# Optimization experiments

Measured on AMD Instinct MI355X. Metric: run time of the kernel, lower is better.

The kernel has to match this reference:

```python
import jax, jax.numpy as jnp
import numpy as np
from jax import lax

ED = 192      # mambapy d_inner = 2 * d_model(Ci=96)
N = 16        # d_state
DT_RANK = 6   # ceil(96/16)
DCONV1 = 4    # mambapy causal conv1d kernel
CI = 96

def _rms(x, w):
    return x * lax.rsqrt(jnp.mean(x * x, axis=-1, keepdims=True) + 1e-5) * w

def _mamba_layer(u, p):
    # u: [B, L, CI]; one mambapy ResidualBlock (RMSNorm -> MambaBlock -> +residual)
    (rms_w, m_in_w, m_conv_w, m_conv_b, x_proj_w, dt_proj_w, dt_proj_b,
     A_log, D_param, m_out_w) = p
    xn = _rms(u, rms_w)
    xz = xn @ m_in_w.T                      # [B,L,2*ED]
    xm, z = jnp.split(xz, 2, axis=-1)
    # causal depthwise conv1d (torch pads d_conv-1 both sides then slices [:L])
    xc = lax.conv_general_dilated(jnp.swapaxes(xm, 1, 2), m_conv_w, (1,),
                                  [(DCONV1 - 1, 0)],
                                  dimension_numbers=('NCH', 'OIH', 'NCH'),
                                  feature_group_count=ED) + m_conv_b[None, :, None]
    xm = jax.nn.silu(jnp.swapaxes(xc, 1, 2))  # [B,L,ED]
    dbc = xm @ x_proj_w.T                     # [B,L,dt_rank+2N]
    dt = dbc[..., :DT_RANK]
    Bm = dbc[..., DT_RANK:DT_RANK + N]
    Cm = dbc[..., DT_RANK + N:]
    delta = jax.nn.softplus(dt @ dt_proj_w.T + dt_proj_b)   # [B,L,ED]
    A = -jnp.exp(A_log)                                      # [ED,N]
    dA = jnp.exp(delta[..., None] * A)                       # [B,L,ED,N]
    dBx = (delta * xm)[..., None] * Bm[:, :, None, :]        # [B,L,ED,N]
    def comb(c1, c2):
        a1, b1 = c1
        a2, b2 = c2
        return a1 * a2, a2 * b1 + b2
    _, h = lax.associative_scan(comb, (dA, dBx), axis=1)     # h: [B,L,ED,N]
    y = jnp.einsum('blen,bln->ble', h, Cm) + D_param * xm
    y = y * jax.nn.silu(z)
    return u + y @ m_out_w.T

def _seq(x3d, p):
    # x3d: [B, C', H, W, D] -> flatten spatial to L, run mamba, reshape back
    B, C, H, W, D = x3d.shape
    xs = jnp.swapaxes(x3d.reshape(B, C, H * W * D), 1, 2)
    ys = _mamba_layer(xs, p)  # mamba_layers = 1
    return jnp.swapaxes(ys, 1, 2).reshape(B, C, H, W, D)

def setup_inputs() -> dict:
    key = jax.random.key(0)
    ks = jax.random.split(key, 12)
    B, H, W, D, C = 1, 16, 16, 16, 96
    s = 0.05
    return {
        'x': jax.random.normal(ks[0], (B, H, W, D, C), jnp.float32),
        'in_proj_w': jax.random.normal(ks[1], (CI, C), jnp.float32) * s,
        'conv3d_w': jax.random.normal(ks[2], (CI, 1, 3, 3, 3), jnp.float32) * s,
        'conv3d_b': jax.random.normal(ks[3], (CI,), jnp.float32) * s,
        'rms_w': jnp.ones((CI,), jnp.float32),
        'm_in_w': jax.random.normal(ks[4], (2 * ED, CI), jnp.float32) * s,
        'm_conv_w': jax.random.normal(ks[5], (ED, 1, DCONV1), jnp.float32) * s,
        'm_conv_b': jax.random.normal(ks[6], (ED,), jnp.float32) * s,
        'x_proj_w': jax.random.normal(ks[7], (DT_RANK + 2 * N, ED), jnp.float32) * s,
        'dt_proj_w': jax.random.normal(ks[8], (ED, DT_RANK), jnp.float32) * s,
        'dt_proj_b': jax.random.uniform(ks[9], (ED,), jnp.float32, -4.0, -2.0),
        'A_log': jnp.log(jnp.tile(jnp.arange(1, N + 1, dtype=jnp.float32), (ED, 1))),
        'D_param': jnp.ones((ED,), jnp.float32),
        'm_out_w': jax.random.normal(ks[10], (CI, ED), jnp.float32) * s,
        'ln_g': jnp.ones((CI,), jnp.float32),
        'ln_b': jnp.zeros((CI,), jnp.float32),
        'out_proj_w': jax.random.normal(ks[11], (C, CI), jnp.float32) * s,
    }

def reference(x, in_proj_w, conv3d_w, conv3d_b, rms_w, m_in_w, m_conv_w, m_conv_b,
              x_proj_w, dt_proj_w, dt_proj_b, A_log, D_param, m_out_w,
              ln_g, ln_b, out_proj_w):
    p = (rms_w, m_in_w, m_conv_w, m_conv_b, x_proj_w, dt_proj_w, dt_proj_b,
         A_log, D_param, m_out_w)
    h = x @ in_proj_w.T                               # [B,H,W,D,Ci]
    xcf = jnp.transpose(h, (0, 4, 1, 2, 3))           # channel-first
    xcf = lax.conv_general_dilated(xcf, conv3d_w, (1, 1, 1), [(1, 1)] * 3,
                                   dimension_numbers=('NCHWD', 'OIHWD', 'NCHWD'),
                                   feature_group_count=CI) \
          + conv3d_b[None, :, None, None, None]
    xcf = jax.nn.silu(xcf)
    x0 = xcf                                          # orientation 0: rot = identity
    x1 = jnp.swapaxes(x0, 2, 4)
    x2 = jnp.swapaxes(x0, 3, 4)
    flip = lambda a: jnp.flip(a, (2, 3, 4))
    y0 = _seq(x0, p) + flip(_seq(flip(x0), p))
    y1 = _seq(x1, p) + flip(_seq(flip(x1), p))
    y2 = _seq(x2, p) + flip(_seq(flip(x2), p))
    y = y0 + jnp.swapaxes(y1, 2, 4) + jnp.swapaxes(y2, 3, 4)
    ycl = jnp.transpose(y, (0, 2, 3, 4, 1))           # channel-last
    mu = jnp.mean(ycl, -1, keepdims=True)
    var = jnp.var(ycl, -1, keepdims=True)
    ycl = (ycl - mu) * lax.rsqrt(var + 1e-5) * ln_g + ln_b
    return ycl @ out_proj_w.T
```

## Files before the change

kernel.cpp:

```cpp
#include <hip/hip_runtime.h>
#include <hip/hip_fp16.h>
#include <math.h>

static constexpr int LSEQ = 4096;
static constexpr int ED_  = 192;
static constexpr int NS   = 16;
static constexpr int NC   = 128;
static constexpr int LC   = 32;
static constexpr int XMS  = 196;
static constexpr int WDS  = 196;

__device__ __forceinline__ float d_silu(float x){ return x / (1.f + __expf(-x)); }
__device__ __forceinline__ float d_softplus(float x){
  return fmaxf(x, 0.f) + __logf(1.f + __expf(-fabsf(x)));
}

__device__ __forceinline__ int vox_of(int l, int ord, int dir){
  int m = dir ? (LSEQ-1-l) : l;
  if(ord==0) return m;
  int a=(m>>8)&15, b=(m>>4)&15, c=m&15;
  if(ord==1) return (c<<8)|(b<<4)|a;
  return (a<<8)|(c<<4)|b;
}

__global__ __launch_bounds__(256) void k_inproj(const float* __restrict__ x, const float* __restrict__ w,
                                                float* __restrict__ hbuf){
  __shared__ float wl[96*104];
  __shared__ float xr[16*100];
  int t = threadIdx.x;
  for(int idx=t; idx<9216; idx+=256){ int o=idx/96, c=idx%96; wl[o*104+c] = w[idx]; }
  int vb = blockIdx.x*16;
  for(int idx=t; idx<1536; idx+=256){ int vv=idx/96, c=idx%96; xr[vv*100+c] = x[(vb+vv)*96 + c]; }
  __syncthreads();
  for(int r=0;r<6;r++){
    int idx = t + 256*r;
    int o = idx>>4, vsub = idx&15;
    const float* xrow = xr + vsub*100;
    const float* wrow = wl + o*104;
    float4 s4 = {0.f,0.f,0.f,0.f};
    #pragma unroll
    for(int c4=0;c4<24;c4++){
      float4 a = *(const float4*)(xrow + c4*4);
      float4 b = *(const float4*)(wrow + c4*4);
      s4.x += a.x*b.x; s4.y += a.y*b.y; s4.z += a.z*b.z; s4.w += a.w*b.w;
    }
    hbuf[(vb+vsub)*96 + o] = (s4.x+s4.y)+(s4.z+s4.w);
  }
}

__global__ __launch_bounds__(256) void k_conv3d(const float* __restrict__ hbuf, const float* __restrict__ w3,
                                                const float* __restrict__ b3, float* __restrict__ x0){
  __shared__ float w3l[96*27];
  __shared__ float b3l[96];
  int t = threadIdx.x;
  for(int idx=t; idx<2592; idx+=256) w3l[idx] = w3[idx];
  if(t<96) b3l[t] = b3[t];
  __syncthreads();
  int idx = blockIdx.x*256 + t;
  int vq = idx/96, c = idx%96;
  int h = vq>>6, wq = (vq>>2)&15, dq = vq&3, d0 = dq*4;
  float acc[4];
  float bb = b3l[c];
  acc[0]=bb; acc[1]=bb; acc[2]=bb; acc[3]=bb;
  for(int i=0;i<3;i++){ int hh=h+i-1; if((unsigned)hh>15u) continue;
    for(int j=0;j<3;j++){ int ww=wq+j-1; if((unsigned)ww>15u) continue;
      float val[6];
      #pragma unroll
      for(int tt=0;tt<6;tt++){
        int dd = d0 + tt - 1;
        val[tt] = ((unsigned)dd<=15u) ? hbuf[(((hh<<4)|ww)<<4|dd)*96 + c] : 0.f;
      }
      const float* wr = w3l + c*27 + i*9 + j*3;
      #pragma unroll
      for(int m=0;m<4;m++)
        acc[m] += val[m]*wr[0] + val[m+1]*wr[1] + val[m+2]*wr[2];
    }}
  int vbase = (((h<<4)|wq)<<4) | d0;
  #pragma unroll
  for(int m=0;m<4;m++) x0[(vbase+m)*96 + c] = d_silu(acc[m]);
}

__global__ __launch_bounds__(256) void k_rms(const float* __restrict__ x0, const float* __restrict__ rms_w,
                                             const float* __restrict__ m_in_w,
                                             float* __restrict__ xmpre, float* __restrict__ szb){
  __shared__ float wl[128*104];
  __shared__ float xn[16*100];
  int t = threadIdx.x;
  int wv = t>>6, lane = t&63;
  int quad = lane>>4, c = lane&15;
  int vsub = wv*4 + quad;
  int v = blockIdx.x*16 + vsub;
  const float* row = x0 + v*96;
  float a[6]; float ssq = 0.f;
  #pragma unroll
  for(int k=0;k<6;k++){ a[k] = row[c+16*k]; ssq += a[k]*a[k]; }
  #pragma unroll
  for(int o=8;o>0;o>>=1) ssq += __shfl_xor(ssq, o, 64);
  float r = rsqrtf(ssq*(1.f/96.f)+1e-5f);
  #pragma unroll
  for(int k=0;k<6;k++) xn[vsub*100 + c + 16*k] = a[k]*r*rms_w[c+16*k];
  for(int tile=0;tile<3;tile++){
    __syncthreads();
    for(int idx=t; idx<12288; idx+=256){ int rr=idx/96, cc=idx%96; wl[rr*104+cc] = m_in_w[(tile*128+rr)*96 + cc]; }
    __syncthreads();
    for(int rpt=0;rpt<8;rpt++){
      int idx = t + 256*rpt;
      int rloc = idx>>4, vs = idx&15;
      int e = tile*128 + rloc;
      const float* xrow = xn + vs*100;
      const float* wrow = wl + rloc*104;
      float4 s4={0.f,0.f,0.f,0.f};
      #pragma unroll
      for(int c4=0;c4<24;c4++){
        float4 aa = *(const float4*)(xrow+c4*4);
        float4 bb = *(const float4*)(wrow+c4*4);
        s4.x+=aa.x*bb.x; s4.y+=aa.y*bb.y; s4.z+=aa.z*bb.z; s4.w+=aa.w*bb.w;
      }
      float dsum = (s4.x+s4.y)+(s4.z+s4.w);
      int vg = blockIdx.x*16 + vs;
      if(e<ED_) xmpre[vg*ED_+e] = dsum;
      else      szb[vg*ED_+(e-ED_)] = d_silu(dsum);
    }
  }
}

__global__ __launch_bounds__(768,6) void kA(
    const float* __restrict__ xmpre,
    const float* __restrict__ mcw, const float* __restrict__ mcb,
    const float* __restrict__ xpw, const float* __restrict__ dtw, const float* __restrict__ dtb,
    const float* __restrict__ Dp,
    __half2* __restrict__ yS, float* __restrict__ hend, float* __restrict__ dbcC){
  __shared__ float s_xm[LC*XMS];
  __shared__ float s_dbc[LC*40];
  __shared__ float s_wdl[38*WDS];
  __shared__ int   vtab[36];
  int s = blockIdx.y, ord = s>>1, dir = s&1;
  int chunk = blockIdx.x, l0 = chunk*LC;
  int tid = threadIdx.x;
  for(int idx=tid; idx<38*192; idx+=768){ int j=idx/192, c=idx-j*192; s_wdl[j*WDS+c] = xpw[idx]; }
  if(tid < 35){
    int l = l0 - 3 + tid;
    vtab[tid] = (l>=0) ? vox_of(l, ord, dir) : 0;
  }
  __syncthreads();
  {
    int g = tid/192, e = tid - g*192;
    float4 wc = *(const float4*)(mcw + e*4);
    float bc = mcb[e];
    int lbase = l0 + 8*g;
    float h0=0.f, h1=0.f, h2=0.f;
    {
      int l = lbase-3; if(l>=0) h0 = xmpre[vtab[8*g+0]*ED_ + e];
      l = lbase-2;     if(l>=0) h1 = xmpre[vtab[8*g+1]*ED_ + e];
      l = lbase-1;     if(l>=0) h2 = xmpre[vtab[8*g+2]*ED_ + e];
    }
    #pragma unroll
    for(int i=0;i<8;i++){
      float cur = xmpre[vtab[8*g+3+i]*ED_ + e];
      float a = bc + h0*wc.x + h1*wc.y + h2*wc.z + cur*wc.w;
      s_xm[(8*g+i)*XMS + e] = d_silu(a);
      h0=h1; h1=h2; h2=cur;
    }
  }
  __syncthreads();
  if(tid < 19*16){
    int jp = tid >> 4;
    int lh = tid & 15;
    int j0 = 2*jp, j1 = 2*jp+1;
    const float4* w40 = (const float4*)(s_wdl + j0*WDS);
    const float4* w41 = (const float4*)(s_wdl + j1*WDS);
    const float4* x4a = (const float4*)(s_xm + lh*XMS);
    const float4* x4b = (const float4*)(s_xm + (lh+16)*XMS);
    float4 sA={0.f,0.f,0.f,0.f}, sB={0.f,0.f,0.f,0.f};
    float4 sC={0.f,0.f,0.f,0.f}, sD={0.f,0.f,0.f,0.f};
    #pragma unroll
    for(int c4=0;c4<48;c4++){
      float4 b0 = w40[c4], b1 = w41[c4];
      float4 aa = x4a[c4];
      sA.x+=aa.x*b0.x; sA.y+=aa.y*b0.y; sA.z+=aa.z*b0.z; sA.w+=aa.w*b0.w;
      sB.x+=aa.x*b1.x; sB.y+=aa.y*b1.y; sB.z+=aa.z*b1.z; sB.w+=aa.w*b1.w;
      float4 ab = x4b[c4];
      sC.x+=ab.x*b0.x; sC.y+=ab.y*b0.y; sC.z+=ab.z*b0.z; sC.w+=ab.w*b0.w;
      sD.x+=ab.x*b1.x; sD.y+=ab.y*b1.y; sD.z+=ab.z*b1.z; sD.w+=ab.w*b1.w;
    }
    int slot0 = (j0<6) ? (32+j0) : (j0-6);
    int slot1 = (j1<6) ? (32+j1) : (j1-6);
    s_dbc[lh*40+slot0]      = (sA.x+sA.y)+(sA.z+sA.w);
    s_dbc[lh*40+slot1]      = (sB.x+sB.y)+(sB.z+sB.w);
    s_dbc[(lh+16)*40+slot0] = (sC.x+sC.y)+(sC.z+sC.w);
    s_dbc[(lh+16)*40+slot1] = (sD.x+sD.y)+(sD.z+sD.w);
  }
  __syncthreads();
  float* s_dl = s_wdl;
  {
    int e = tid % ED_, g = tid / ED_;
    float wdt0=dtw[e*6+0], wdt1=dtw[e*6+1], wdt2=dtw[e*6+2];
    float wdt3=dtw[e*6+3], wdt4=dtw[e*6+4], wdt5=dtw[e*6+5];
    float bdt = dtb[e];
    #pragma unroll
    for(int p=0;p<8;p++){
      int lc = g + 4*p;
      const float* db = s_dbc + lc*40 + 32;
      float a = bdt + db[0]*wdt0 + db[1]*wdt1 + db[2]*wdt2 + db[3]*wdt3 + db[4]*wdt4 + db[5]*wdt5;
      s_dl[lc*ED_ + e] = d_softplus(a);
    }
  }
  for(int idx=tid; idx<LC*16; idx+=768){
    int l = idx>>4, n = idx&15;
    dbcC[(s*LSEQ + l0 + l)*16 + n] = s_dbc[l*40 + 16 + n];
  }
  __syncthreads();
  if(tid < 384){
    int e = tid>>1, q = tid&1, n0 = q*8;
    float De = Dp[e];
    float h[8] = {0.f,0.f,0.f,0.f,0.f,0.f,0.f,0.f};
    float Srun = 0.f;
    for(int lc=0; lc<LC; lc++){
      float dl = s_dl[lc*ED_ + e];
      float xm = s_xm[lc*XMS + e];
      const float* db = s_dbc + lc*40;
      float4 Bv0 = *(const float4*)(db + n0);
      float4 Bv1 = *(const float4*)(db + n0 + 4);
      float4 Cv0 = *(const float4*)(db + 16 + n0);
      float4 Cv1 = *(const float4*)(db + 16 + n0 + 4);
      float dxm = dl*xm;
      float r  = __expf(-dl);
      float r2 = r*r, r4 = r2*r2, r8 = r4*r4;
      float a = q ? (r8*r) : r;
      float py;
      h[0] = a*h[0] + dxm*Bv0.x; py  = h[0]*Cv0.x; a *= r;
      h[1] = a*h[1] + dxm*Bv0.y; py += h[1]*Cv0.y; a *= r;
      h[2] = a*h[2] + dxm*Bv0.z; py += h[2]*Cv0.z; a *= r;
      h[3] = a*h[3] + dxm*Bv0.w; py += h[3]*Cv0.w; a *= r;
      h[4] = a*h[4] + dxm*Bv1.x; py += h[4]*Cv1.x; a *= r;
      h[5] = a*h[5] + dxm*Bv1.y; py += h[5]*Cv1.y; a *= r;
      h[6] = a*h[6] + dxm*Bv1.z; py += h[6]*Cv1.z; a *= r;
      h[7] = a*h[7] + dxm*Bv1.w; py += h[7]*Cv1.w;
      py += __shfl_xor(py,1,64);
      if(q==0){
        Srun += dl;
        int l = l0+lc;
        yS[(s*LSEQ+l)*ED_+e] = __floats2half2_rn(py + De*xm, Srun);
      }
    }
    int base = (s*NC+chunk)*(ED_*NS) + e*NS + n0;
    float4 hv0 = {h[0],h[1],h[2],h[3]};
    float4 hv1 = {h[4],h[5],h[6],h[7]};
    *(float4*)(hend + base)     = hv0;
    *(float4*)(hend + base + 4) = hv1;
  }
}

__global__ __launch_bounds__(256) void kB(const __half2* __restrict__ yS, float* hend){
  int t = blockIdx.x*256 + threadIdx.x;
  int s = t/(ED_*NS), st = t - s*(ED_*NS);
  int e = st>>4, n = st&15;
  float A = -(float)(n+1);
  float h = 0.f;
  float Sv[8], bv[8], Sn[8], bn[8];
  #pragma unroll
  for(int j=0;j<8;j++){
    Sv[j] = __high2float(yS[(s*LSEQ + j*LC + (LC-1))*ED_ + e]);
    bv[j] = hend[(s*NC + j)*(ED_*NS) + st];
  }
  for(int blk=0; blk<16; blk++){
    if(blk<15){
      #pragma unroll
      for(int j=0;j<8;j++){
        int c = (blk+1)*8 + j;
        Sn[j] = __high2float(yS[(s*LSEQ + c*LC + (LC-1))*ED_ + e]);
        bn[j] = hend[(s*NC + c)*(ED_*NS) + st];
      }
    }
    #pragma unroll
    for(int j=0;j<8;j++){
      float a = __expf(A*Sv[j]);
      hend[(s*NC + blk*8+j)*(ED_*NS) + st] = h;
      h = a*h + bv[j];
    }
    #pragma unroll
    for(int j=0;j<8;j++){ Sv[j]=Sn[j]; bv[j]=bn[j]; }
  }
}

__global__ __launch_bounds__(768) void k_corr2(const float* __restrict__ dbcC, const float* __restrict__ hstart,
                                               const __half2* __restrict__ yS, __half* __restrict__ yh){
  __shared__ float sC[LC*16];
  int s = blockIdx.y, chunk = blockIdx.x, l0 = chunk*LC;
  int tid = threadIdx.x;
  if(tid < 512) sC[tid] = dbcC[(s*LSEQ+l0)*16 + tid];
  int g = tid/192, e = tid - g*192;
  const float4* Hp = (const float4*)(hstart + (s*NC+chunk)*(ED_*NS) + e*16);
  float4 H0 = Hp[0], H1 = Hp[1], H2 = Hp[2], H3 = Hp[3];
  __syncthreads();
  #pragma unroll
  for(int i=0;i<8;i++){
    int lc = g*8 + i;
    int base = (s*LSEQ + l0 + lc)*ED_ + e;
    __half2 p = yS[base];
    float yl = __low2float(p), S = __high2float(p);
    float t1 = __expf(-S);
    const float* Cr = sC + lc*16;
    float pw = t1, corr = pw*H0.x*Cr[0];
    pw*=t1; corr+=pw*H0.y*Cr[1];
    pw*=t1; corr+=pw*H0.z*Cr[2];
    pw*=t1; corr+=pw*H0.w*Cr[3];
    pw*=t1; corr+=pw*H1.x*Cr[4];
    pw*=t1; corr+=pw*H1.y*Cr[5];
    pw*=t1; corr+=pw*H1.z*Cr[6];
    pw*=t1; corr+=pw*H1.w*Cr[7];
    pw*=t1; corr+=pw*H2.x*Cr[8];
    pw*=t1; corr+=pw*H2.y*Cr[9];
    pw*=t1; corr+=pw*H2.z*Cr[10];
    pw*=t1; corr+=pw*H2.w*Cr[11];
    pw*=t1; corr+=pw*H3.x*Cr[12];
    pw*=t1; corr+=pw*H3.y*Cr[13];
    pw*=t1; corr+=pw*H3.z*Cr[14];
    pw*=t1; corr+=pw*H3.w*Cr[15];
    yh[base] = __float2half(yl + corr);
  }
}

__global__ __launch_bounds__(384) void k_out(const __half* __restrict__ yh,
                                             const float* __restrict__ szb, const float* __restrict__ x0,
                                             const float* __restrict__ mow,
                                             const float* __restrict__ ln_g, const float* __restrict__ ln_b,
                                             const float* __restrict__ opw, float* __restrict__ out){
  __shared__ float smem[12000];
  float* ys   = smem;
  float* wl   = smem + 1568;
  float* accl = smem + 11168;
  int t = threadIdx.x;
  int vb = blockIdx.x*8;
  for(int rr=0; rr<4; rr++){
    int idx = t + 384*rr;
    int vsub = idx/192, e = idx%192;
    int v = vb + vsub;
    float ssum = 0.f;
    #pragma unroll
    for(int s=0;s<6;s++){
      int l = vox_of(v, s>>1, s&1);
      ssum += __half2float(yh[(s*LSEQ+l)*ED_ + e]);
    }
    ys[vsub*196+e] = ssum * szb[v*ED_+e];
  }
  for(int half=0; half<2; half++){
    __syncthreads();
    for(int idx=t; idx<9216; idx+=384){ int co=idx/192, c=idx%192; wl[co*196+c] = mow[(half*48+co)*192 + c]; }
    __syncthreads();
    int col = t>>3, vs = t&7;
    const float4* y4 = (const float4*)(ys + vs*196);
    const float4* w4 = (const float4*)(wl + col*196);
    float4 s4={0.f,0.f,0.f,0.f};
    #pragma unroll
    for(int c4=0;c4<48;c4++){
      float4 a=y4[c4], b=w4[c4];
      s4.x+=a.x*b.x; s4.y+=a.y*b.y; s4.z+=a.z*b.z; s4.w+=a.w*b.w;
    }
    int v = vb + vs, co = half*48 + col;
    accl[vs*104+co] = 6.f*x0[v*96+co] + (s4.x+s4.y)+(s4.z+s4.w);
  }
  __syncthreads();
  for(int idx=t; idx<9216; idx+=384){ int o=idx/96, c=idx%96; wl[o*100+c] = opw[idx]; }
  float* ynorm = ys;
  if(t < 256){
    int wv = t>>6, lane = t&63;
    int half = lane>>5, c = lane&31;
    int vsub = wv*2 + half;
    const float* row = accl + vsub*104;
    float a0=row[c], a1=row[c+32], a2=row[c+64];
    float s1 = a0+a1+a2, s2 = a0*a0+a1*a1+a2*a2;
    #pragma unroll
    for(int o=16;o>0;o>>=1){ s1+=__shfl_xor(s1,o,64); s2+=__shfl_xor(s2,o,64); }
    float mean = s1*(1.f/96.f);
    float var = s2*(1.f/96.f) - mean*mean;
    float r = rsqrtf(var+1e-5f);
    ynorm[vsub*100+c]    = (a0-mean)*r*ln_g[c]+ln_b[c];
    ynorm[vsub*100+c+32] = (a1-mean)*r*ln_g[c+32]+ln_b[c+32];
    ynorm[vsub*100+c+64] = (a2-mean)*r*ln_g[c+64]+ln_b[c+64];
  }
  __syncthreads();
  for(int rr=0;rr<2;rr++){
    int idx = t+384*rr;
    int o = idx>>3, vs = idx&7;
    const float* ya = ynorm+vs*100;
    const float* wrow = wl+o*100;
    float4 s4={0.f,0.f,0.f,0.f};
    #pragma unroll
    for(int c4=0;c4<24;c4++){
      float4 a=*(const float4*)(ya+c4*4), b=*(const float4*)(wrow+c4*4);
      s4.x+=a.x*b.x; s4.y+=a.y*b.y; s4.z+=a.z*b.z; s4.w+=a.w*b.w;
    }
    out[(vb+vs)*96+o] = (s4.x+s4.y)+(s4.z+s4.w);
  }
}

extern "C" void kernel_launch(void* const* d_in, const int* in_sizes, int n_in,
                              void* d_out, int out_size, void* d_ws, size_t ws_size,
                              hipStream_t stream){
  (void)in_sizes; (void)n_in; (void)out_size; (void)ws_size;
  const float* x         = (const float*)d_in[0];
  const float* in_proj_w = (const float*)d_in[1];
  const float* conv3d_w  = (const float*)d_in[2];
  const float* conv3d_b  = (const float*)d_in[3];
  const float* rms_w     = (const float*)d_in[4];
  const float* m_in_w    = (const float*)d_in[5];
  const float* m_conv_w  = (const float*)d_in[6];
  const float* m_conv_b  = (const float*)d_in[7];
  const float* x_proj_w  = (const float*)d_in[8];
  const float* dt_proj_w = (const float*)d_in[9];
  const float* dt_proj_b = (const float*)d_in[10];
  const float* D_param   = (const float*)d_in[12];
  const float* m_out_w   = (const float*)d_in[13];
  const float* ln_g      = (const float*)d_in[14];
  const float* ln_bb     = (const float*)d_in[15];
  const float* out_proj_w= (const float*)d_in[16];
  float* out = (float*)d_out;

  float* ws    = (float*)d_ws;
  float* hbuf  = ws;
  float* x0    = ws + 393216;
  float* xmpre = ws + 786432;
  float* szb   = ws + 1572864;
  __half2* yS  = (__half2*)(ws + 2756608);
  __half*  yh  = (__half*) (ws + 7475200);
  float* hend  = ws + 12193792;
  float* dbcC  = hbuf;

  k_inproj<<<256,256,0,stream>>>(x, in_proj_w, hbuf);
  k_conv3d<<<384,256,0,stream>>>(hbuf, conv3d_w, conv3d_b, x0);
  k_rms<<<256,256,0,stream>>>(x0, rms_w, m_in_w, xmpre, szb);
  dim3 g(NC, 6);
  kA<<<g,768,0,stream>>>(xmpre, m_conv_w, m_conv_b, x_proj_w, dt_proj_w, dt_proj_b,
                         D_param, yS, hend, dbcC);
  kB<<<72,256,0,stream>>>(yS, hend);
  k_corr2<<<g,768,0,stream>>>(dbcC, hend, yS, yh);
  k_out<<<512,384,0,stream>>>(yh, szb, x0, m_out_w, ln_g, ln_bb, out_proj_w, out);
}
```

Measured before the change: 119.2 us.

## Double scan chunk length, store activations in fp16, enlarge per-block tiles

Measured after the change: 138.1 us. +15.9%, slower.

```diff
diff --git a/kernel.cpp b/kernel.cpp
--- a/kernel.cpp
+++ b/kernel.cpp
@@ -5,10 +5,20 @@
 static constexpr int LSEQ = 4096;
 static constexpr int ED_  = 192;
 static constexpr int NS   = 16;
-static constexpr int NC   = 128;
-static constexpr int LC   = 32;
-static constexpr int XMS  = 196;
-static constexpr int WDS  = 196;
+static constexpr int NC   = 64;
+static constexpr int LC   = 64;
+static constexpr int XMS2 = 200;
+
+typedef _Float16 h2v __attribute__((ext_vector_type(2)));
+
+#if defined(__has_builtin)
+#if __has_builtin(__builtin_amdgcn_fdot2)
+#define FDOT2(a,b,c) __builtin_amdgcn_fdot2((a),(b),(c),false)
+#endif
+#endif
+#ifndef FDOT2
+#define FDOT2(a,b,c) ((c) + (float)(a).x*(float)(b).x + (float)(a).y*(float)(b).y)
+#endif
 
 __device__ __forceinline__ float d_silu(float x){ return x / (1.f + __expf(-x)); }
 __device__ __forceinline__ float d_softplus(float x){
@@ -26,15 +36,15 @@
 __global__ __launch_bounds__(256) void k_inproj(const float* __restrict__ x, const float* __restrict__ w,
                                                 float* __restrict__ hbuf){
   __shared__ float wl[96*104];
-  __shared__ float xr[16*100];
+  __shared__ float xr[32*100];
   int t = threadIdx.x;
   for(int idx=t; idx<9216; idx+=256){ int o=idx/96, c=idx%96; wl[o*104+c] = w[idx]; }
-  int vb = blockIdx.x*16;
-  for(int idx=t; idx<1536; idx+=256){ int vv=idx/96, c=idx%96; xr[vv*100+c] = x[(vb+vv)*96 + c]; }
-  __syncthreads();
-  for(int r=0;r<6;r++){
+  int vb = blockIdx.x*32;
+  for(int idx=t; idx<3072; idx+=256){ int vv=idx/96, c=idx%96; xr[vv*100+c] = x[(vb+vv)*96 + c]; }
+  __syncthreads();
+  for(int r=0;r<12;r++){
     int idx = t + 256*r;
-    int o = idx>>4, vsub = idx&15;
+    int o = idx>>5, vsub = idx&31;
     const float* xrow = xr + vsub*100;
     const float* wrow = wl + o*104;
     float4 s4 = {0.f,0.f,0.f,0.f};
@@ -84,28 +94,31 @@
                                              const float* __restrict__ m_in_w,
                                              float* __restrict__ xmpre, float* __restrict__ szb){
   __shared__ float wl[128*104];
-  __shared__ float xn[16*100];
+  __shared__ float xn[32*100];
   int t = threadIdx.x;
   int wv = t>>6, lane = t&63;
   int quad = lane>>4, c = lane&15;
-  int vsub = wv*4 + quad;
-  int v = blockIdx.x*16 + vsub;
-  const float* row = x0 + v*96;
-  float a[6]; float ssq = 0.f;
-  #pragma unroll
-  for(int k=0;k<6;k++){ a[k] = row[c+16*k]; ssq += a[k]*a[k]; }
-  #pragma unroll
-  for(int o=8;o>0;o>>=1) ssq += __shfl_xor(ssq, o, 64);
-  float r = rsqrtf(ssq*(1.f/96.f)+1e-5f);
-  #pragma unroll
-  for(int k=0;k<6;k++) xn[vsub*100 + c + 16*k] = a[k]*r*rms_w[c+16*k];
+  int vsub0 = wv*4 + quad;
+  for(int hh=0; hh<2; hh++){
+    int vsub = vsub0 + 16*hh;
+    int v = blockIdx.x*32 + vsub;
+    const float* row = x0 + v*96;
+    float a[6]; float ssq = 0.f;
+    #pragma unroll
+    for(int k=0;k<6;k++){ a[k] = row[c+16*k]; ssq += a[k]*a[k]; }
+    #pragma unroll
+    for(int o=8;o>0;o>>=1) ssq += __shfl_xor(ssq, o, 64);
+    float r = rsqrtf(ssq*(1.f/96.f)+1e-5f);
+    #pragma unroll
+    for(int k=0;k<6;k++) xn[vsub*100 + c + 16*k] = a[k]*r*rms_w[c+16*k];
+  }
   for(int tile=0;tile<3;tile++){
     __syncthreads();
     for(int idx=t; idx<12288; idx+=256){ int rr=idx/96, cc=idx%96; wl[rr*104+cc] = m_in_w[(tile*128+rr)*96 + cc]; }
     __syncthreads();
-    for(int rpt=0;rpt<8;rpt++){
+    for(int rpt=0;rpt<16;rpt++){
       int idx = t + 256*rpt;
-      int rloc = idx>>4, vs = idx&15;
+      int rloc = idx>>5, vs = idx&31;
       int e = tile*128 + rloc;
       const float* xrow = xn + vs*100;
       const float* wrow = wl + rloc*104;
@@ -117,7 +130,7 @@
         s4.x+=aa.x*bb.x; s4.y+=aa.y*bb.y; s4.z+=aa.z*bb.z; s4.w+=aa.w*bb.w;
       }
       float dsum = (s4.x+s4.y)+(s4.z+s4.w);
-      int vg = blockIdx.x*16 + vs;
+      int vg = blockIdx.x*32 + vs;
       if(e<ED_) xmpre[vg*ED_+e] = dsum;
       else      szb[vg*ED_+(e-ED_)] = d_silu(dsum);
     }
@@ -130,15 +143,16 @@
     const float* __restrict__ xpw, const float* __restrict__ dtw, const float* __restrict__ dtb,
     const float* __restrict__ Dp,
     __half2* __restrict__ yS, float* __restrict__ hend, float* __restrict__ dbcC){
-  __shared__ float s_xm[LC*XMS];
+  __shared__ _Float16 s_xm[LC*XMS2];
+  __shared__ _Float16 s_u[LC*XMS2];
   __shared__ float s_dbc[LC*40];
-  __shared__ float s_wdl[38*WDS];
-  __shared__ int   vtab[36];
+  __shared__ int   vtab[LC+3];
   int s = blockIdx.y, ord = s>>1, dir = s&1;
   int chunk = blockIdx.x, l0 = chunk*LC;
   int tid = threadIdx.x;
-  for(int idx=tid; idx<38*192; idx+=768){ int j=idx/192, c=idx-j*192; s_wdl[j*WDS+c] = xpw[idx]; }
-  if(tid < 35){
+  _Float16* s_wdl = s_u;
+  for(int idx=tid; idx<38*192; idx+=768){ int j=idx/192, c=idx-j*192; s_wdl[j*XMS2+c] = (_Float16)xpw[idx]; }
+  if(tid < LC+3){
     int l = l0 - 3 + tid;
     vtab[tid] = (l>=0) ? vox_of(l, ord, dir) : 0;
   }
@@ -147,67 +161,68 @@
     int g = tid/192, e = tid - g*192;
     float4 wc = *(const float4*)(mcw + e*4);
     float bc = mcb[e];
-    int lbase = l0 + 8*g;
+    int j0 = 16*g;
+    int lbase = l0 + 16*g;
     float h0=0.f, h1=0.f, h2=0.f;
-    {
-      int l = lbase-3; if(l>=0) h0 = xmpre[vtab[8*g+0]*ED_ + e];
-      l = lbase-2;     if(l>=0) h1 = xmpre[vtab[8*g+1]*ED_ + e];
-      l = lbase-1;     if(l>=0) h2 = xmpre[vtab[8*g+2]*ED_ + e];
-    }
-    #pragma unroll
-    for(int i=0;i<8;i++){
-      float cur = xmpre[vtab[8*g+3+i]*ED_ + e];
+    if(lbase-3>=0) h0 = xmpre[vtab[j0+0]*ED_ + e];
+    if(lbase-2>=0) h1 = xmpre[vtab[j0+1]*ED_ + e];
+    if(lbase-1>=0) h2 = xmpre[vtab[j0+2]*ED_ + e];
+    #pragma unroll
+    for(int i=0;i<16;i++){
+      float cur = xmpre[vtab[j0+3+i]*ED_ + e];
       float a = bc + h0*wc.x + h1*wc.y + h2*wc.z + cur*wc.w;
-      s_xm[(8*g+i)*XMS + e] = d_silu(a);
+      s_xm[(16*g+i)*XMS2 + e] = (_Float16)d_silu(a);
       h0=h1; h1=h2; h2=cur;
     }
   }
   __syncthreads();
-  if(tid < 19*16){
-    int jp = tid >> 4;
-    int lh = tid & 15;
-    int j0 = 2*jp, j1 = 2*jp+1;
-    const float4* w40 = (const float4*)(s_wdl + j0*WDS);
-    const float4* w41 = (const float4*)(s_wdl + j1*WDS);
-    const float4* x4a = (const float4*)(s_xm + lh*XMS);
-    const float4* x4b = (const float4*)(s_xm + (lh+16)*XMS);
-    float4 sA={0.f,0.f,0.f,0.f}, sB={0.f,0.f,0.f,0.f};
-    float4 sC={0.f,0.f,0.f,0.f}, sD={0.f,0.f,0.f,0.f};
-    #pragma unroll
-    for(int c4=0;c4<48;c4++){
-      float4 b0 = w40[c4], b1 = w41[c4];
-      float4 aa = x4a[c4];
-      sA.x+=aa.x*b0.x; sA.y+=aa.y*b0.y; sA.z+=aa.z*b0.z; sA.w+=aa.w*b0.w;
-      sB.x+=aa.x*b1.x; sB.y+=aa.y*b1.y; sB.z+=aa.z*b1.z; sB.w+=aa.w*b1.w;
-      float4 ab = x4b[c4];
-      sC.x+=ab.x*b0.x; sC.y+=ab.y*b0.y; sC.z+=ab.z*b0.z; sC.w+=ab.w*b0.w;
-      sD.x+=ab.x*b1.x; sD.y+=ab.y*b1.y; sD.z+=ab.z*b1.z; sD.w+=ab.w*b1.w;
+  if(tid < 19*32){
+    int jp = tid >> 5;
+    int lh = tid & 31;
+    int j0 = 2*jp, j1 = j0+1;
+    const float4* w40 = (const float4*)(s_wdl + j0*XMS2);
+    const float4* w41 = (const float4*)(s_wdl + j1*XMS2);
+    const float4* x4a = (const float4*)(s_xm + lh*XMS2);
+    const float4* x4b = (const float4*)(s_xm + (lh+32)*XMS2);
+    float sA=0.f, sB=0.f, sC=0.f, sD=0.f;
+    #pragma unroll
+    for(int c4=0;c4<24;c4++){
+      float4 wa = w40[c4], wb = w41[c4], xa = x4a[c4], xb = x4b[c4];
+      const h2v* pwa=(const h2v*)&wa; const h2v* pwb=(const h2v*)&wb;
+      const h2v* pxa=(const h2v*)&xa; const h2v* pxb=(const h2v*)&xb;
+      #pragma unroll
+      for(int k=0;k<4;k++){
+        sA = FDOT2(pxa[k], pwa[k], sA);
+        sB = FDOT2(pxa[k], pwb[k], sB);
+        sC = FDOT2(pxb[k], pwa[k], sC);
+        sD = FDOT2(pxb[k], pwb[k], sD);
+      }
     }
     int slot0 = (j0<6) ? (32+j0) : (j0-6);
     int slot1 = (j1<6) ? (32+j1) : (j1-6);
-    s_dbc[lh*40+slot0]      = (sA.x+sA.y)+(sA.z+sA.w);
-    s_dbc[lh*40+slot1]      = (sB.x+sB.y)+(sB.z+sB.w);
-    s_dbc[(lh+16)*40+slot0] = (sC.x+sC.y)+(sC.z+sC.w);
-    s_dbc[(lh+16)*40+slot1] = (sD.x+sD.y)+(sD.z+sD.w);
-  }
-  __syncthreads();
-  float* s_dl = s_wdl;
+    s_dbc[lh*40+slot0]      = sA;
+    s_dbc[lh*40+slot1]      = sB;
+    s_dbc[(lh+32)*40+slot0] = sC;
+    s_dbc[(lh+32)*40+slot1] = sD;
+  }
+  __syncthreads();
+  for(int idx=tid; idx<LC*16; idx+=768){
+    int l = idx>>4, n = idx&15;
+    dbcC[(s*LSEQ + l0 + l)*16 + n] = s_dbc[l*40 + 16 + n];
+  }
+  _Float16* s_dl = s_u;
   {
     int e = tid % ED_, g = tid / ED_;
     float wdt0=dtw[e*6+0], wdt1=dtw[e*6+1], wdt2=dtw[e*6+2];
     float wdt3=dtw[e*6+3], wdt4=dtw[e*6+4], wdt5=dtw[e*6+5];
     float bdt = dtb[e];
     #pragma unroll
-    for(int p=0;p<8;p++){
+    for(int p=0;p<16;p++){
       int lc = g + 4*p;
       const float* db = s_dbc + lc*40 + 32;
       float a = bdt + db[0]*wdt0 + db[1]*wdt1 + db[2]*wdt2 + db[3]*wdt3 + db[4]*wdt4 + db[5]*wdt5;
-      s_dl[lc*ED_ + e] = d_softplus(a);
-    }
-  }
-  for(int idx=tid; idx<LC*16; idx+=768){
-    int l = idx>>4, n = idx&15;
-    dbcC[(s*LSEQ + l0 + l)*16 + n] = s_dbc[l*40 + 16 + n];
+      s_dl[lc*XMS2 + e] = (_Float16)d_softplus(a);
+    }
   }
   __syncthreads();
   if(tid < 384){
@@ -216,8 +231,8 @@
     float h[8] = {0.f,0.f,0.f,0.f,0.f,0.f,0.f,0.f};
     float Srun = 0.f;
     for(int lc=0; lc<LC; lc++){
-      float dl = s_dl[lc*ED_ + e];
-      float xm = s_xm[lc*XMS + e];
+      float dl = (float)s_dl[lc*XMS2 + e];
+      float xm = (float)s_xm[lc*XMS2 + e];
       const float* db = s_dbc + lc*40;
       float4 Bv0 = *(const float4*)(db + n0);
       float4 Bv1 = *(const float4*)(db + n0 + 4);
@@ -239,8 +254,7 @@
       py += __shfl_xor(py,1,64);
       if(q==0){
         Srun += dl;
-        int l = l0+lc;
-        yS[(s*LSEQ+l)*ED_+e] = __floats2half2_rn(py + De*xm, Srun);
+        yS[(s*LSEQ + l0 + lc)*ED_+e] = __floats2half2_rn(py + De*xm, Srun);
       }
     }
     int base = (s*NC+chunk)*(ED_*NS) + e*NS + n0;
@@ -263,8 +277,8 @@
     Sv[j] = __high2float(yS[(s*LSEQ + j*LC + (LC-1))*ED_ + e]);
     bv[j] = hend[(s*NC + j)*(ED_*NS) + st];
   }
-  for(int blk=0; blk<16; blk++){
-    if(blk<15){
+  for(int blk=0; blk<8; blk++){
+    if(blk<7){
       #pragma unroll
       for(int j=0;j<8;j++){
         int c = (blk+1)*8 + j;
@@ -288,14 +302,14 @@
   __shared__ float sC[LC*16];
   int s = blockIdx.y, chunk = blockIdx.x, l0 = chunk*LC;
   int tid = threadIdx.x;
-  if(tid < 512) sC[tid] = dbcC[(s*LSEQ+l0)*16 + tid];
+  for(int idx=tid; idx<LC*16; idx+=768) sC[idx] = dbcC[(s*LSEQ+l0)*16 + idx];
   int g = tid/192, e = tid - g*192;
   const float4* Hp = (const float4*)(hstart + (s*NC+chunk)*(ED_*NS) + e*16);
   float4 H0 = Hp[0], H1 = Hp[1], H2 = Hp[2], H3 = Hp[3];
   __syncthreads();
   #pragma unroll
-  for(int i=0;i<8;i++){
-    int lc = g*8 + i;
+  for(int i=0;i<16;i++){
+    int lc = g*16 + i;
     int base = (s*LSEQ + l0 + lc)*ED_ + e;
     __half2 p = yS[base];
     float yl = __low2float(p), S = __high2float(p);
@@ -326,13 +340,13 @@
                                              const float* __restrict__ mow,
                                              const float* __restrict__ ln_g, const float* __restrict__ ln_b,
                                              const float* __restrict__ opw, float* __restrict__ out){
-  __shared__ float smem[12000];
+  __shared__ float smem[14400];
   float* ys   = smem;
-  float* wl   = smem + 1568;
-  float* accl = smem + 11168;
+  float* wl   = smem + 3136;
+  float* accl = smem + 12736;
   int t = threadIdx.x;
-  int vb = blockIdx.x*8;
-  for(int rr=0; rr<4; rr++){
+  int vb = blockIdx.x*16;
+  for(int rr=0; rr<8; rr++){
     int idx = t + 384*rr;
     int vsub = idx/192, e = idx%192;
     int v = vb + vsub;
@@ -348,41 +362,47 @@
     __syncthreads();
     for(int idx=t; idx<9216; idx+=384){ int co=idx/192, c=idx%192; wl[co*196+c] = mow[(half*48+co)*192 + c]; }
     __syncthreads();
-    int col = t>>3, vs = t&7;
-    const float4* y4 = (const float4*)(ys + vs*196);
-    const float4* w4 = (const float4*)(wl + col*196);
-    float4 s4={0.f,0.f,0.f,0.f};
-    #pragma unroll
-    for(int c4=0;c4<48;c4++){
-      float4 a=y4[c4], b=w4[c4];
-      s4.x+=a.x*b.x; s4.y+=a.y*b.y; s4.z+=a.z*b.z; s4.w+=a.w*b.w;
-    }
-    int v = vb + vs, co = half*48 + col;
-    accl[vs*104+co] = 6.f*x0[v*96+co] + (s4.x+s4.y)+(s4.z+s4.w);
+    for(int rp=0; rp<2; rp++){
+      int idx = t + 384*rp;
+      int col = idx>>4, vs = idx&15;
+      const float4* y4 = (const float4*)(ys + vs*196);
+      const float4* w4 = (const float4*)(wl + col*196);
+      float4 s4={0.f,0.f,0.f,0.f};
+      #pragma unroll
+      for(int c4=0;c4<48;c4++){
+        float4 a=y4[c4], b=w4[c4];
+        s4.x+=a.x*b.x; s4.y+=a.y*b.y; s4.z+=a.z*b.z; s4.w+=a.w*b.w;
+      }
+      int v = vb + vs, co = half*48 + col;
+      accl[vs*104+co] = 6.f*x0[v*96+co] + (s4.x+s4.y)+(s4.z+s4.w);
+    }
   }
   __syncthreads();
   for(int idx=t; idx<9216; idx+=384){ int o=idx/96, c=idx%96; wl[o*100+c] = opw[idx]; }
   float* ynorm = ys;
-  if(t < 256){
+  {
     int wv = t>>6, lane = t&63;
-    int half = lane>>5, c = lane&31;
-    int vsub = wv*2 + half;
-    const float* row = accl + vsub*104;
-    float a0=row[c], a1=row[c+32], a2=row[c+64];
-    float s1 = a0+a1+a2, s2 = a0*a0+a1*a1+a2*a2;
-    #pragma unroll
-    for(int o=16;o>0;o>>=1){ s1+=__shfl_xor(s1,o,64); s2+=__shfl_xor(s2,o,64); }
-    float mean = s1*(1.f/96.f);
-    float var = s2*(1.f/96.f) - mean*mean;
-    float r = rsqrtf(var+1e-5f);
-    ynorm[vsub*100+c]    = (a0-mean)*r*ln_g[c]+ln_b[c];
-    ynorm[vsub*100+c+32] = (a1-mean)*r*ln_g[c+32]+ln_b[c+32];
-    ynorm[vsub*100+c+64] = (a2-mean)*r*ln_g[c+64]+ln_b[c+64];
-  }
-  __syncthreads();
-  for(int rr=0;rr<2;rr++){
+    int quad = lane>>4, c = lane&15;
+    int vsub = wv*4 + quad;
+    if(vsub < 16){
+      const float* row = accl + vsub*104;
+      float a[6]; float s1=0.f, s2=0.f;
+      #pragma unroll
+      for(int k=0;k<6;k++){ a[k]=row[c+16*k]; s1+=a[k]; s2+=a[k]*a[k]; }
+      #pragma unroll
+      for(int o=8;o>0;o>>=1){ s1+=__shfl_xor(s1,o,64); s2+=__shfl_xor(s2,o,64); }
+      float mean = s1*(1.f/96.f);
+      float var = s2*(1.f/96.f) - mean*mean;
+      float r = rsqrtf(var+1e-5f);
+      #pragma unroll
+      for(int k=0;k<6;k++)
+        ynorm[vsub*100+c+16*k] = (a[k]-mean)*r*ln_g[c+16*k]+ln_b[c+16*k];
+    }
+  }
+  __syncthreads();
+  for(int rr=0;rr<4;rr++){
     int idx = t+384*rr;
-    int o = idx>>3, vs = idx&7;
+    int o = idx>>4, vs = idx&15;
     const float* ya = ynorm+vs*100;
     const float* wrow = wl+o*100;
     float4 s4={0.f,0.f,0.f,0.f};
@@ -427,13 +447,13 @@
   float* hend  = ws + 12193792;
   float* dbcC  = hbuf;
 
-  k_inproj<<<256,256,0,stream>>>(x, in_proj_w, hbuf);
+  k_inproj<<<128,256,0,stream>>>(x, in_proj_w, hbuf);
   k_conv3d<<<384,256,0,stream>>>(hbuf, conv3d_w, conv3d_b, x0);
-  k_rms<<<256,256,0,stream>>>(x0, rms_w, m_in_w, xmpre, szb);
+  k_rms<<<128,256,0,stream>>>(x0, rms_w, m_in_w, xmpre, szb);
   dim3 g(NC, 6);
   kA<<<g,768,0,stream>>>(xmpre, m_conv_w, m_conv_b, x_proj_w, dt_proj_w, dt_proj_b,
                          D_param, yS, hend, dbcC);
   kB<<<72,256,0,stream>>>(yS, hend);
   k_corr2<<<g,768,0,stream>>>(dbcC, hend, yS, yh);
-  k_out<<<512,384,0,stream>>>(yh, szb, x0, m_out_w, ln_g, ln_bb, out_proj_w, out);
-}
+  k_out<<<256,384,0,stream>>>(yh, szb, x0, m_out_w, ln_g, ln_bb, out_proj_w, out);
+}
```
